# Optimization experiments

Measured on AMD Instinct MI355X. Metric: run time of the kernel, lower is better.

Reference implementation:

```python
import jax, jax.numpy as jnp
import numpy as np

# config
BSZ, L_, DM = 4, 2048, 1024
H, G, P, N, R = 16, 4, 64, 64, 2
RATIO = H // G            # 4
E, K = 64, 2              # kmoe experts / top_k
DPROJ = H * P * 2 + G * N * R * 2 + G * 3  # 3084


def rms(x, w, eps=1e-5):
    return x * jax.lax.rsqrt(jnp.mean(x * x, axis=-1, keepdims=True) + eps) * w


def kron_moe(x, router_w, A_e, B_e, scale, bias, d1, d2, o1, o2, k):
    # x: [..., d1*d2] -> [..., o1*o2]
    orig = x.shape
    xf = x.reshape(-1, d1 * d2)
    logits = xf @ router_w.T                       # [T, E]
    vals, idx = jax.lax.top_k(logits, k)           # [T, k]
    probs = jax.nn.softmax(vals, axis=-1)
    xs = xf.reshape(-1, d1, d2)
    # Y[t,k,o,p] = sum_ij A[t,k,o,i] x[t,i,j] B[t,k,p,j]
    Y = jnp.einsum('tkoi,tij,tkpj->tkop', A_e[idx], xs, B_e[idx])
    out = jnp.sum(Y * probs[:, :, None, None], axis=1).reshape(orig[:-1] + (o1 * o2,))
    return out * scale + bias


def setup_inputs() -> dict:
    key = jax.random.key(0)
    ks = jax.random.split(key, 12)
    r = lambda k, s, sc: jax.random.normal(k, s, jnp.float32) * sc
    return dict(
        u=jax.random.normal(ks[0], (BSZ, L_, DM), jnp.float32),
        in_proj_w=r(ks[1], (DPROJ, DM), 0.02),
        in_proj_b=jnp.zeros((DPROJ,), jnp.float32),
        xup_router=r(ks[2], (E, P), 0.02),
        xup_A=r(ks[3], (E, 8, 8), 0.1),
        xup_B=r(ks[4], (E, 16, 8), 0.1),
        xup_scale=jnp.ones((1,), jnp.float32),
        xup_bias=jnp.zeros((P * R,), jnp.float32),
        ydown_w=r(ks[5], (P, P * R), 0.02),
        oup_router=r(ks[6], (E, H * P), 0.02),
        oup_A=r(ks[7], (E, 32, 32), 0.05),
        oup_B=r(ks[8], (E, 32, 32), 0.05),
        oup_scale=jnp.ones((1,), jnp.float32),
        oup_bias=jnp.zeros((DM,), jnp.float32),
        theta_log=r(ks[9], (G, N // 2), 1.0),
        D=jnp.ones((H,), jnp.float32),
        normB_w=jnp.ones((N * R,), jnp.float32),
        normC_w=jnp.ones((N * R,), jnp.float32),
        bias_B=jnp.zeros((G, N, R), jnp.float32),
        bias_C=jnp.zeros((G, N, R), jnp.float32),
        pregate_w=jnp.ones((H * P,), jnp.float32),
    )


def reference(u, in_proj_w, in_proj_b, xup_router, xup_A, xup_B, xup_scale, xup_bias,
              ydown_w, oup_router, oup_A, oup_B, oup_scale, oup_bias,
              theta_log, D, normB_w, normC_w, bias_B, bias_C, pregate_w):
    B, L, _ = u.shape
    HP, GNR = H * P, G * N * R
    proj = u @ in_proj_w.T + in_proj_b
    splits = np.cumsum([HP, HP, GNR, GNR, G, G])
    z, x_p, Bp, Cp, dt, A_p, lam = jnp.split(proj, splits, axis=-1)
    dt = jax.nn.softplus(dt)                       # [B,L,G]
    A = -jnp.exp(A_p)                              # [B,L,G]
    theta = jnp.exp(theta_log)                     # [G,N/2]
    Bp = rms(Bp.reshape(B, L, G, N * R), normB_w).reshape(B, L, G, N, R) + bias_B
    Cp = rms(Cp.reshape(B, L, G, N * R), normC_w).reshape(B, L, G, N, R) + bias_C
    angles_g = jnp.cumsum(dt[..., None] * theta[None, None], axis=1)   # [B,L,G,N/2]
    rep = lambda v: jnp.repeat(v, RATIO, axis=2)   # group -> head broadcast
    angles = rep(angles_g)                         # [B,L,H,N/2]
    dt_h = rep(dt[..., None])                      # [B,L,H,1]
    A_h = rep(A[..., None])                        # [B,L,H,1]
    B_h, C_h = rep(Bp), rep(Cp)                    # [B,L,H,N,R]
    cos = jnp.cos(angles)[..., None]
    sin = jnp.sin(angles)[..., None]

    def rotate(v):
        re, im = v[..., 0::2, :], v[..., 1::2, :]
        return jnp.stack([re * cos - im * sin, re * sin + im * cos], axis=-2).reshape(v.shape)

    B_rot, C_rot = rotate(B_h), rotate(C_h)
    x = kron_moe(x_p.reshape(B, L, H, P), xup_router, xup_A, xup_B, xup_scale, xup_bias,
                 8, 8, 8, 16, K).reshape(B, L, H, P, R)
    alpha = jnp.exp(dt_h * A_h)[..., None]         # [B,L,H,1,1]

    mv = lambda v: jnp.moveaxis(v, 1, 0)           # time-major for scan

    def step(h, xs):
        Br, Cr, xt, at, dtt = xs
        in_sig = jnp.einsum('bhnr,bhpr->bhnp', Br, xt)
        h = h * at + dtt[..., None] * in_sig
        y_t = jnp.einsum('bhnp,bhnr->bhpr', h, Cr)
        return h, y_t

    h0 = jnp.zeros((B, H, N, P), u.dtype)
    _, ys = jax.lax.scan(step, h0, (mv(B_rot), mv(C_rot), mv(x), mv(alpha), mv(dt_h)))
    y = jnp.moveaxis(ys, 0, 1)                     # [B,L,H,P,R]
    y = (y.reshape(B, L, H, P * R) @ ydown_w.T).reshape(B, L, H * P)
    y = rms(y + x_p * jnp.repeat(D, P), pregate_w) * jax.nn.sigmoid(z)
    out = kron_moe(y, oup_router, oup_A, oup_B, oup_scale, oup_bias, 32, 32, 32, 32, K)
    return out
```

## Files before the change

### kernel.cpp

```cpp
#include <hip/hip_runtime.h>
#include <hip/hip_bf16.h>
#include <math.h>

namespace {
constexpr int kB = 4, kL = 2048, kDM = 1024;
constexpr int kH = 16, kG = 4;
constexpr int kDPROJ = 3084;
constexpr int COL_Z = 0, COL_XP = 1024, COL_B = 2048, COL_C = 2560, COL_DT = 3072, COL_A = 3076;
constexpr int kTOK = kB * kL;
constexpr int kNC = kL / 64;
constexpr int kNPAD = 3200;
constexpr float kLOG2E = 1.4426950408889634f;
}

typedef __attribute__((ext_vector_type(8))) __bf16 bf16x8;
typedef __attribute__((ext_vector_type(8))) unsigned short u16x8;
typedef __attribute__((ext_vector_type(4))) float f32x4;

#define GLDS16(gp, lp)                                                          \
  __builtin_amdgcn_global_load_lds(                                             \
      (const __attribute__((address_space(1))) void*)(gp),                      \
      (__attribute__((address_space(3))) void*)(lp), 16, 0, 0)

__device__ __forceinline__ unsigned short bf16_rne(float f) {
  unsigned u = __builtin_bit_cast(unsigned, f);
  unsigned r = u + 0x7fffu + ((u >> 16) & 1u);
  return (unsigned short)(r >> 16);
}
__device__ __forceinline__ void split2(float f, unsigned short& h, unsigned short& l) {
  unsigned short hh = bf16_rne(f);
  float hf = __builtin_bit_cast(float, (unsigned)hh << 16);
  h = hh;
  l = bf16_rne(f - hf);
}
__device__ __forceinline__ bf16x8 ldsb8(const unsigned short* p) {
  return __builtin_bit_cast(bf16x8, *(const u16x8*)p);
}

__global__ __launch_bounds__(256) void k_split_u(const float* __restrict__ X,
                                                 unsigned short* __restrict__ hi,
                                                 unsigned short* __restrict__ lo) {
  int i = blockIdx.x * 256 + threadIdx.x;
  float4 x = ((const float4*)X)[i];
  float xs[4] = {x.x, x.y, x.z, x.w};
  ushort4 hv, lv;
  unsigned short hq[4], lq[4];
#pragma unroll
  for (int q = 0; q < 4; ++q) split2(xs[q], hq[q], lq[q]);
  hv.x = hq[0]; hv.y = hq[1]; hv.z = hq[2]; hv.w = hq[3];
  lv.x = lq[0]; lv.y = lq[1]; lv.z = lq[2]; lv.w = lq[3];
  ((ushort4*)hi)[i] = hv;
  ((ushort4*)lo)[i] = lv;
}

__global__ __launch_bounds__(256) void k_split_w(const float* __restrict__ X,
                                                 unsigned short* __restrict__ hi,
                                                 unsigned short* __restrict__ lo) {
  int i = blockIdx.x * 256 + threadIdx.x;
  int row = i >> 8;
  float4 x = make_float4(0.f, 0.f, 0.f, 0.f);
  if (row < kDPROJ) x = ((const float4*)X)[i];
  float xs[4] = {x.x, x.y, x.z, x.w};
  ushort4 hv, lv;
  unsigned short hq[4], lq[4];
#pragma unroll
  for (int q = 0; q < 4; ++q) split2(xs[q], hq[q], lq[q]);
  hv.x = hq[0]; hv.y = hq[1]; hv.z = hq[2]; hv.w = hq[3];
  lv.x = lq[0]; lv.y = lq[1]; lv.z = lq[2]; lv.w = lq[3];
  ((ushort4*)hi)[i] = hv;
  ((ushort4*)lo)[i] = lv;
}

__global__ __launch_bounds__(256) void k_inproj_mfma(
    const unsigned short* __restrict__ Uhi, const unsigned short* __restrict__ Ulo,
    const unsigned short* __restrict__ Whi, const unsigned short* __restrict__ Wlo,
    const float* __restrict__ bias, float* __restrict__ proj) {
  __shared__ unsigned short lds_u[16384];
  const int tid = threadIdx.x;
  const int wave = tid >> 6, lane = tid & 63;
  const int wm = wave >> 1, wn = wave & 1;
  const int row0 = blockIdx.x * 128, col0 = blockIdx.y * 128;
  const int fr = lane & 15, kq = lane >> 4;

  f32x4 acc[4][4];
#pragma unroll
  for (int i = 0; i < 4; ++i)
#pragma unroll
    for (int j = 0; j < 4; ++j) acc[i][j] = (f32x4){0.f, 0.f, 0.f, 0.f};

  const int s0 = wave * 64 + lane;

  for (int k0 = 0; k0 < kDM; k0 += 32) {
#pragma unroll
    for (int q = 0; q < 2; ++q) {
      const int slot = q * 256 + s0;
      const int r = slot >> 2;
      const int ce = ((slot & 3) ^ ((r >> 1) & 3)) * 8;
      const size_t ao = (size_t)(row0 + r) * kDM + k0 + ce;
      const size_t bo = (size_t)(col0 + r) * kDM + k0 + ce;
      const int lb = (q * 256 + wave * 64) * 16;
      GLDS16(Uhi + ao, (char*)lds_u + lb);
      GLDS16(Ulo + ao, (char*)lds_u + 8192 + lb);
      GLDS16(Whi + bo, (char*)lds_u + 16384 + lb);
      GLDS16(Wlo + bo, (char*)lds_u + 24576 + lb);
    }
    __syncthreads();
    bf16x8 ahi[4], alo[4], bhi[4], blo[4];
#pragma unroll
    for (int mi = 0; mi < 4; ++mi) {
      int r = wm * 64 + mi * 16 + fr;
      int off = r * 32 + ((kq ^ ((r >> 1) & 3)) * 8);
      ahi[mi] = ldsb8(lds_u + off);
      alo[mi] = ldsb8(lds_u + 4096 + off);
    }
#pragma unroll
    for (int ni = 0; ni < 4; ++ni) {
      int r = wn * 64 + ni * 16 + fr;
      int off = r * 32 + ((kq ^ ((r >> 1) & 3)) * 8);
      bhi[ni] = ldsb8(lds_u + 8192 + off);
      blo[ni] = ldsb8(lds_u + 12288 + off);
    }
#pragma unroll
    for (int mi = 0; mi < 4; ++mi)
#pragma unroll
      for (int ni = 0; ni < 4; ++ni) {
        acc[mi][ni] = __builtin_amdgcn_mfma_f32_16x16x32_bf16(ahi[mi], bhi[ni], acc[mi][ni], 0, 0, 0);
        acc[mi][ni] = __builtin_amdgcn_mfma_f32_16x16x32_bf16(ahi[mi], blo[ni], acc[mi][ni], 0, 0, 0);
        acc[mi][ni] = __builtin_amdgcn_mfma_f32_16x16x32_bf16(alo[mi], bhi[ni], acc[mi][ni], 0, 0, 0);
      }
    __syncthreads();
  }

  const int orow = row0 + wm * 64, ocol = col0 + wn * 64;
#pragma unroll
  for (int mi = 0; mi < 4; ++mi)
#pragma unroll
    for (int ni = 0; ni < 4; ++ni) {
      int cg = ocol + ni * 16 + fr;
      if (cg < kDPROJ) {
        float bv = bias[cg];
#pragma unroll
        for (int r = 0; r < 4; ++r) {
          int rg = orow + mi * 16 + kq * 4 + r;
          proj[(size_t)rg * kDPROJ + cg] = acc[mi][ni][r] + bv;
        }
      }
    }
}

__global__ __launch_bounds__(256) void k_dtprep(const float* __restrict__ proj,
                                                float* __restrict__ dtg,
                                                float* __restrict__ cumalog,
                                                double* __restrict__ cumdt) {
  int bg = blockIdx.x;
  int b = bg / kG, g = bg % kG;
  int tid = threadIdx.x;
  __shared__ double s_dt[256], s_al[256];
  double loc_dt[8], loc_al[8];
  double sdt = 0.0, sal = 0.0;
#pragma unroll
  for (int q = 0; q < 8; ++q) {
    int t = tid * 8 + q;
    size_t i = (size_t)(b * kL + t) * kDPROJ;
    float rd = proj[i + COL_DT + g];
    float ra = proj[i + COL_A + g];
    float dt = rd > 20.f ? rd : log1pf(expf(rd));
    float al = -expf(ra) * dt;
    dtg[(size_t)(b * kL + t) * kG + g] = dt;
    sdt += (double)dt; loc_dt[q] = sdt;
    sal += (double)al; loc_al[q] = sal;
  }
  s_dt[tid] = sdt; s_al[tid] = sal;
  __syncthreads();
  for (int off = 1; off < 256; off <<= 1) {
    double a = 0.0, c = 0.0;
    if (tid >= off) { a = s_dt[tid - off]; c = s_al[tid - off]; }
    __syncthreads();
    s_dt[tid] += a; s_al[tid] += c;
    __syncthreads();
  }
  double base_dt = tid ? s_dt[tid - 1] : 0.0;
  double base_al = tid ? s_al[tid - 1] : 0.0;
#pragma unroll
  for (int q = 0; q < 8; ++q) {
    int t = tid * 8 + q;
    size_t idx = (size_t)(b * kL + t) * kG + g;
    cumdt[idx] = base_dt + loc_dt[q];
    cumalog[idx] = (float)(base_al + loc_al[q]);
  }
}

__global__ __launch_bounds__(256) void k_angles(const double* __restrict__ cumdt,
                                                const float* __restrict__ theta_log,
                                                float* __restrict__ cs_tab) {
  int idx = blockIdx.x * 256 + threadIdx.x;
  int tok = idx >> 7, gk = idx & 127, g = gk >> 5, k = gk & 31;
  double theta = exp((double)theta_log[g * 32 + k]);
  double ang = theta * cumdt[(size_t)tok * kG + g];
  const double twopi = 6.283185307179586476925286766559;
  double rem = ang - floor(ang / twopi) * twopi;
  cs_tab[(size_t)idx * 2] = cosf((float)rem);
  cs_tab[(size_t)idx * 2 + 1] = sinf((float)rem);
}

__global__ __launch_bounds__(256) void k_rotate(float* __restrict__ proj,
                                                const float* __restrict__ cs_tab,
                                                const float* __restrict__ normB_w,
                                                const float* __restrict__ normC_w,
                                                const float* __restrict__ bias_B,
                                                const float* __restrict__ bias_C) {
  int tok = blockIdx.x;
  int tid = threadIdx.x;
  __shared__ float buf[256];
  __shared__ float red[4];
  size_t rowoff = (size_t)tok * kDPROJ;
  int half = tid >> 7;
  int j = tid & 127;
  int wave = tid >> 6;
  for (int g = 0; g < kG; ++g) {
    int col = (half ? COL_C : COL_B) + g * 128 + j;
    float v = proj[rowoff + col];
    float ss = v * v;
    for (int o = 1; o < 64; o <<= 1) ss += __shfl_xor(ss, o);
    if ((tid & 63) == 0) red[wave] = ss;
    __syncthreads();
    float tot = red[half * 2] + red[half * 2 + 1];
    float scale = rsqrtf(tot / 128.f + 1e-5f);
    const float* nw = half ? normC_w : normB_w;
    const float* bb = half ? bias_C : bias_B;
    float nv = v * scale * nw[j] + bb[g * 128 + j];
    buf[tid] = nv;
    __syncthreads();
    float other = buf[tid ^ 2];
    int n = j >> 1, k = n >> 1;
    bool isRe = (n & 1) == 0;
    const float* cs = cs_tab + (((size_t)tok * kG + g) * 32 + k) * 2;
    float cc = cs[0], sn = cs[1];
    float out = isRe ? (nv * cc - other * sn) : (other * sn + nv * cc);
    proj[rowoff + col] = out;
    __syncthreads();
  }
}

__global__ __launch_bounds__(256) void k_xup(const float* __restrict__ proj,
                                             const float* __restrict__ router,
                                             const float* __restrict__ Ae,
                                             const float* __restrict__ Be,
                                             const float* __restrict__ scale_,
                                             const float* __restrict__ bias_,
                                             float* __restrict__ xmoe) {
  int wave = threadIdx.x >> 6, lane = threadIdx.x & 63;
  int unit = blockIdx.x * 4 + wave;
  int tok = unit >> 4, h = unit & 15;
  __shared__ float xs_all[4][64];
  __shared__ float Rs[64][65];
  for (int m = threadIdx.x; m < 64 * 64; m += 256) Rs[m >> 6][m & 63] = router[m];
  float xv = proj[(size_t)tok * kDPROJ + COL_XP + h * 64 + lane];
  xs_all[wave][lane] = xv;
  __syncthreads();
  const float* xs = xs_all[wave];
  double accd = 0.0;
#pragma unroll
  for (int d = 0; d < 64; ++d) accd += (double)Rs[lane][d] * (double)xs[d];
  float logit = (float)accd;
  float v1 = logit; int i1 = lane;
  for (int o = 1; o < 64; o <<= 1) {
    float vv = __shfl_xor(v1, o); int ii = __shfl_xor(i1, o);
    if (vv > v1 || (vv == v1 && ii < i1)) { v1 = vv; i1 = ii; }
  }
  float lm = (lane == i1) ? -INFINITY : logit;
  float v2 = lm; int i2 = lane;
  for (int o = 1; o < 64; o <<= 1) {
    float vv = __shfl_xor(v2, o); int ii = __shfl_xor(i2, o);
    if (vv > v2 || (vv == v2 && ii < i2)) { v2 = vv; i2 = ii; }
  }
  float e12 = expf(v2 - v1);
  float p1 = 1.f / (1.f + e12), p2 = e12 / (1.f + e12);
  float out0 = 0.f, out1 = 0.f;
#pragma unroll
  for (int kk = 0; kk < 2; ++kk) {
    int e = kk ? i2 : i1;
    float pw = kk ? p2 : p1;
    const float* A = Ae + (size_t)e * 64;
    const float* Bm = Be + (size_t)e * 128;
#pragma unroll
    for (int hlf = 0; hlf < 2; ++hlf) {
      int c = lane + hlf * 64;
      int o = c >> 4, p = c & 15;
      float y = 0.f;
#pragma unroll
      for (int i = 0; i < 8; ++i) {
        float t = 0.f;
#pragma unroll
        for (int jj = 0; jj < 8; ++jj) t += xs[i * 8 + jj] * Bm[p * 8 + jj];
        y += A[o * 8 + i] * t;
      }
      if (hlf) out1 += pw * y; else out0 += pw * y;
    }
  }
  float sc = scale_[0];
  size_t ob = (size_t)unit * 128;
  xmoe[ob + lane] = out0 * sc + bias_[lane];
  xmoe[ob + lane + 64] = out1 * sc + bias_[lane + 64];
}

__global__ __launch_bounds__(256) void k_passA(const float* __restrict__ proj,
                                               const float* __restrict__ xmoe,
                                               const float* __restrict__ dtg,
                                               const float* __restrict__ cumalog,
                                               float* __restrict__ hstate) {
  int bid = blockIdx.x;
  int c = bid & 31, h = (bid >> 5) & 15, b = bid >> 9, g = h >> 2;
  int tid = threadIdx.x;
  __shared__ float Bs[128][65];
  __shared__ float Xs[128][65];
  __shared__ float wv[64];
  int base = c * 64;
  size_t tok0 = (size_t)b * kL + base;
  if (tid < 64) {
    float ca_last = cumalog[(tok0 + 63) * kG + g];
    float ca_s = cumalog[(tok0 + tid) * kG + g];
    float dt = dtg[(tok0 + tid) * kG + g];
    wv[tid] = expf(ca_last - ca_s) * dt;
  }
  __syncthreads();
  for (int m = tid; m < 8192; m += 256) {
    int s = m >> 7, j = m & 127;
    float bval = proj[(tok0 + s) * kDPROJ + COL_B + g * 128 + j];
    Bs[s * 2 + (j & 1)][j >> 1] = bval * wv[s];
    float xval = xmoe[((tok0 + s) * kH + h) * (size_t)128 + j];
    Xs[s * 2 + (j & 1)][j >> 1] = xval;
  }
  __syncthreads();
  int tx = tid & 15, ty = tid >> 4;
  float acc[4][4];
#pragma unroll
  for (int i = 0; i < 4; ++i)
#pragma unroll
    for (int j = 0; j < 4; ++j) acc[i][j] = 0.f;
  for (int k = 0; k < 128; ++k) {
    float a[4], bv[4];
#pragma unroll
    for (int q = 0; q < 4; ++q) a[q] = Bs[k][ty * 4 + q];
#pragma unroll
    for (int q = 0; q < 4; ++q) bv[q] = Xs[k][tx * 4 + q];
#pragma unroll
    for (int i = 0; i < 4; ++i)
#pragma unroll
      for (int j = 0; j < 4; ++j) acc[i][j] += a[i] * bv[j];
  }
  float* out = hstate + (size_t)bid * 4096;
#pragma unroll
  for (int i = 0; i < 4; ++i)
#pragma unroll
    for (int j = 0; j < 4; ++j)
      out[(ty * 4 + i) * 64 + tx * 4 + j] = acc[i][j];
}

__global__ __launch_bounds__(256) void k_passB(float* __restrict__ hstate,
                                               const float* __restrict__ cumalog) {
  int bh = blockIdx.x;
  int b = bh >> 4, h = bh & 15, g = h >> 2;
  int tid = threadIdx.x;
  float hrun[16];
#pragma unroll
  for (int q = 0; q < 16; ++q) hrun[q] = 0.f;
  float* Hbase = hstate + (size_t)bh * 32 * 4096;
  for (int c = 0; c < 32; ++c) {
    float ca_last = cumalog[((size_t)b * kL + c * 64 + 63) * kG + g];
    float ca_prev = c ? cumalog[((size_t)b * kL + c * 64 - 1) * kG + g] : 0.f;
    float Dc = expf(ca_last - ca_prev);
    float* Hc = Hbase + (size_t)c * 4096;
#pragma unroll
    for (int q = 0; q < 16; ++q) {
      int idx = tid + q * 256;
      float local = Hc[idx];
      Hc[idx] = hrun[q];
      hrun[q] = Dc * hrun[q] + local;
    }
  }
}

namespace {
constexpr int SC = 72;
constexpr int SG = 136;
constexpr int SH = 72;
constexpr int SW = 66;
}
__global__ __launch_bounds__(256) void k_passC(const float* __restrict__ proj,
                                               const float* __restrict__ xmoe,
                                               const float* __restrict__ dtg,
                                               const float* __restrict__ cumalog,
                                               const float* __restrict__ hstate,
                                               const float* __restrict__ ydown,
                                               float* __restrict__ outY) {
  __shared__ __align__(16) char smem[162560];
  unsigned short* sCh = (unsigned short*)smem;
  unsigned short* sCl = sCh + 128 * SC;
  unsigned short* sBh = (unsigned short*)(smem + 36864);
  unsigned short* sBl = sBh + 128 * SC;
  float*          sW  = (float*)(smem + 73728);
  unsigned short* sHh = (unsigned short*)(smem + 73728);
  unsigned short* sHl = sHh + 64 * SH;
  unsigned short* sGh = (unsigned short*)(smem + 92160);
  unsigned short* sGl = sGh + 128 * SG;
  float* sca  = (float*)(smem + 161792);
  float* sdts = sca + 64;
  float* selx = sdts + 64;
  unsigned short* sXh  = (unsigned short*)smem;
  unsigned short* sXl  = sXh + 64 * SG;
  unsigned short* sWdh = (unsigned short*)(smem + 36864);
  unsigned short* sWdl = sWdh + 64 * SG;
  unsigned short* sYh  = (unsigned short*)(smem + 92160);
  unsigned short* sYl  = sYh + 64 * SG;

  int bid = blockIdx.x;
  int c = bid & 31, h = (bid >> 5) & 15, b = bid >> 9, g = h >> 2;
  int tid = threadIdx.x;
  const int wave = tid >> 6, lane = tid & 63;
  const int fr = lane & 15, kq = lane >> 4;
  int base = c * 64;
  size_t tok0 = (size_t)b * kL + base;
  size_t projBase = tok0 * kDPROJ;

  if (tid < 64) {
    float ca_prev = base ? cumalog[(tok0 - 1) * kG + g] : 0.f;
    float ca_t = cumalog[(tok0 + tid) * kG + g];
    sca[tid] = ca_t;
    sdts[tid] = dtg[(tok0 + tid) * kG + g];
    selx[tid] = exp2f((ca_t - ca_prev) * kLOG2E);
  }
  for (int m = tid; m < 8192; m += 256) {
    int s = m >> 7, j = m & 127;
    int row = s * 2 + (j & 1), col = j >> 1;
    unsigned short hh, ll;
    float cv = proj[projBase + (size_t)s * kDPROJ + COL_C + g * 128 + j];
    split2(cv, hh, ll);
    sCh[row * SC + col] = hh; sCl[row * SC + col] = ll;
    float bv = proj[projBase + (size_t)s * kDPROJ + COL_B + g * 128 + j];
    split2(bv, hh, ll);
    sBh[row * SC + col] = hh; sBl[row * SC + col] = ll;
  }
  __syncthreads();

  for (int m = tid; m < 4096; m += 256) {
    int t = m >> 6, s = m & 63;
    float w = (s <= t) ? sdts[s] * exp2f((sca[t] - sca[s]) * kLOG2E) : 0.f;
    sW[t * SW + s] = w;
  }
  const int rowA0 = wave * 32;
  f32x4 gacc[2][8];
#pragma unroll
  for (int i = 0; i < 2; ++i)
#pragma unroll
    for (int j = 0; j < 8; ++j) gacc[i][j] = (f32x4){0.f, 0.f, 0.f, 0.f};
#pragma unroll
  for (int ks = 0; ks < 2; ++ks) {
    int kb = ks * 32 + kq * 8;
    bf16x8 ah[2], al[2];
#pragma unroll
    for (int mi = 0; mi < 2; ++mi) {
      int off = (rowA0 + mi * 16 + fr) * SC + kb;
      ah[mi] = ldsb8(sCh + off);
      al[mi] = ldsb8(sCl + off);
    }
#pragma unroll
    for (int ni = 0; ni < 8; ++ni) {
      int off = (ni * 16 + fr) * SC + kb;
      bf16x8 bh = ldsb8(sBh + off);
      bf16x8 bl = ldsb8(sBl + off);
#pragma unroll
      for (int mi = 0; mi < 2; ++mi) {
        gacc[mi][ni] = __builtin_amdgcn_mfma_f32_16x16x32_bf16(ah[mi], bh, gacc[mi][ni], 0, 0, 0);
        gacc[mi][ni] = __builtin_amdgcn_mfma_f32_16x16x32_bf16(ah[mi], bl, gacc[mi][ni], 0, 0, 0);
        gacc[mi][ni] = __builtin_amdgcn_mfma_f32_16x16x32_bf16(al[mi], bh, gacc[mi][ni], 0, 0, 0);
      }
    }
  }
  __syncthreads();

#pragma unroll
  for (int mi = 0; mi < 2; ++mi)
#pragma unroll
    for (int ni = 0; ni < 8; ++ni) {
      int colg = ni * 16 + fr;
      int s = colg >> 1;
#pragma unroll
      for (int r = 0; r < 4; ++r) {
        int rowg = rowA0 + mi * 16 + kq * 4 + r;
        int t = rowg >> 1;
        float gm = gacc[mi][ni][r] * sW[t * SW + s];
        unsigned short hh, ll;
        split2(gm, hh, ll);
        sGh[rowg * SG + colg] = hh;
        sGl[rowg * SG + colg] = ll;
      }
    }
  __syncthreads();

  for (int m = tid; m < 4096; m += 256) {
    int n = m >> 6, p = m & 63;
    float v = hstate[(size_t)bid * 4096 + m];
    unsigned short hh, ll;
    split2(v, hh, ll);
    sHh[p * SH + n] = hh;
    sHl[p * SH + n] = ll;
  }
  __syncthreads();

  f32x4 yac[2][4];
#pragma unroll
  for (int i = 0; i < 2; ++i)
#pragma unroll
    for (int j = 0; j < 4; ++j) yac[i][j] = (f32x4){0.f, 0.f, 0.f, 0.f};
#pragma unroll
  for (int ks = 0; ks < 2; ++ks) {
    int kb = ks * 32 + kq * 8;
    bf16x8 ah[2], al[2];
#pragma unroll
    for (int mi = 0; mi < 2; ++mi) {
      int off = (rowA0 + mi * 16 + fr) * SC + kb;
      ah[mi] = ldsb8(sCh + off);
      al[mi] = ldsb8(sCl + off);
    }
#pragma unroll
    for (int ni = 0; ni < 4; ++ni) {
      int off = (ni * 16 + fr) * SH + kb;
      bf16x8 bh = ldsb8(sHh + off);
      bf16x8 bl = ldsb8(sHl + off);
#pragma unroll
      for (int mi = 0; mi < 2; ++mi) {
        yac[mi][ni] = __builtin_amdgcn_mfma_f32_16x16x32_bf16(ah[mi], bh, yac[mi][ni], 0, 0, 0);
        yac[mi][ni] = __builtin_amdgcn_mfma_f32_16x16x32_bf16(ah[mi], bl, yac[mi][ni], 0, 0, 0);
        yac[mi][ni] = __builtin_amdgcn_mfma_f32_16x16x32_bf16(al[mi], bh, yac[mi][ni], 0, 0, 0);
      }
    }
  }
#pragma unroll
  for (int mi = 0; mi < 2; ++mi)
#pragma unroll
    for (int r = 0; r < 4; ++r) {
      int t = (rowA0 + mi * 16 + kq * 4 + r) >> 1;
      float e = selx[t];
#pragma unroll
      for (int ni = 0; ni < 4; ++ni) yac[mi][ni][r] *= e;
    }
  __syncthreads();

  for (int m = tid; m < 8192; m += 256) {
    int s = m >> 7, j = m & 127;
    float xv = xmoe[((tok0 + s) * kH + h) * (size_t)128 + j];
    int p = j >> 1, cc = s * 2 + (j & 1);
    unsigned short hh, ll;
    split2(xv, hh, ll);
    sXh[p * SG + cc] = hh; sXl[p * SG + cc] = ll;
    float wv = ydown[m];
    split2(wv, hh, ll);
    sWdh[(m >> 7) * SG + (m & 127)] = hh;
    sWdl[(m >> 7) * SG + (m & 127)] = ll;
  }
  __syncthreads();

#pragma unroll
  for (int ks = 0; ks < 4; ++ks) {
    int kb = ks * 32 + kq * 8;
    bf16x8 ah[2], al[2];
#pragma unroll
    for (int mi = 0; mi < 2; ++mi) {
      int off = (rowA0 + mi * 16 + fr) * SG + kb;
      ah[mi] = ldsb8(sGh + off);
      al[mi] = ldsb8(sGl + off);
    }
#pragma unroll
    for (int ni = 0; ni < 4; ++ni) {
      int off = (ni * 16 + fr) * SG + kb;
      bf16x8 bh = ldsb8(sXh + off);
      bf16x8 bl = ldsb8(sXl + off);
#pragma unroll
      for (int mi = 0; mi < 2; ++mi) {
        yac[mi][ni] = __builtin_amdgcn_mfma_f32_16x16x32_bf16(ah[mi], bh, yac[mi][ni], 0, 0, 0);
        yac[mi][ni] = __builtin_amdgcn_mfma_f32_16x16x32_bf16(ah[mi], bl, yac[mi][ni], 0, 0, 0);
        yac[mi][ni] = __builtin_amdgcn_mfma_f32_16x16x32_bf16(al[mi], bh, yac[mi][ni], 0, 0, 0);
      }
    }
  }
  __syncthreads();

#pragma unroll
  for (int mi = 0; mi < 2; ++mi)
#pragma unroll
    for (int ni = 0; ni < 4; ++ni)
#pragma unroll
      for (int r = 0; r < 4; ++r) {
        int rowg = rowA0 + mi * 16 + kq * 4 + r;
        int t = rowg >> 1, rr = rowg & 1;
        int p = ni * 16 + fr;
        unsigned short hh, ll;
        split2(yac[mi][ni][r], hh, ll);
        sYh[t * SG + p * 2 + rr] = hh;
        sYl[t * SG + p * 2 + rr] = ll;
      }
  __syncthreads();

  f32x4 zac[4];
#pragma unroll
  for (int j = 0; j < 4; ++j) zac[j] = (f32x4){0.f, 0.f, 0.f, 0.f};
#pragma unroll
  for (int ks = 0; ks < 4; ++ks) {
    int kb = ks * 32 + kq * 8;
    int offA = (wave * 16 + fr) * SG + kb;
    bf16x8 ah = ldsb8(sYh + offA);
    bf16x8 al = ldsb8(sYl + offA);
#pragma unroll
    for (int ni = 0; ni < 4; ++ni) {
      int off = (ni * 16 + fr) * SG + kb;
      bf16x8 bh = ldsb8(sWdh + off);
      bf16x8 bl = ldsb8(sWdl + off);
      zac[ni] = __builtin_amdgcn_mfma_f32_16x16x32_bf16(ah, bh, zac[ni], 0, 0, 0);
      zac[ni] = __builtin_amdgcn_mfma_f32_16x16x32_bf16(ah, bl, zac[ni], 0, 0, 0);
      zac[ni] = __builtin_amdgcn_mfma_f32_16x16x32_bf16(al, bh, zac[ni], 0, 0, 0);
    }
  }
#pragma unroll
  for (int ni = 0; ni < 4; ++ni)
#pragma unroll
    for (int r = 0; r < 4; ++r) {
      int t = wave * 16 + kq * 4 + r;
      int o = ni * 16 + fr;
      outY[(tok0 + t) * (size_t)1024 + h * 64 + o] = zac[ni][r];
    }
}

__global__ __launch_bounds__(256) void k_gate(float* __restrict__ y,
                                              const float* __restrict__ proj,
                                              const float* __restrict__ Dv,
                                              const float* __restrict__ pregate_w) {
  int tok = blockIdx.x;
  int tid = threadIdx.x;
  size_t yoff = (size_t)tok * 1024;
  size_t poff = (size_t)tok * kDPROJ;
  __shared__ float red[4];
  float vals[4];
  float ss = 0.f;
#pragma unroll
  for (int q = 0; q < 4; ++q) {
    int j = tid + q * 256;
    float v = y[yoff + j] + proj[poff + COL_XP + j] * Dv[j >> 6];
    vals[q] = v;
    ss += v * v;
  }
  for (int o = 1; o < 64; o <<= 1) ss += __shfl_xor(ss, o);
  if ((tid & 63) == 0) red[tid >> 6] = ss;
  __syncthreads();
  float tot = red[0] + red[1] + red[2] + red[3];
  float scale = rsqrtf(tot / 1024.f + 1e-5f);
#pragma unroll
  for (int q = 0; q < 4; ++q) {
    int j = tid + q * 256;
    float z = proj[poff + COL_Z + j];
    float sig = 1.f / (1.f + expf(-z));
    y[yoff + j] = vals[q] * scale * pregate_w[j] * sig;
  }
}

__global__ __launch_bounds__(256) void k_oup(float* __restrict__ y,
                                             const float* __restrict__ router,
                                             const float* __restrict__ Ae,
                                             const float* __restrict__ Be,
                                             const float* __restrict__ scale_,
                                             const float* __restrict__ bias_) {
  int tok = blockIdx.x;
  int tid = threadIdx.x;
  __shared__ float xs[1024];
  __shared__ float Ts[32][33];
  __shared__ float logits_s[64];
  __shared__ double partial[256];
  size_t yoff = (size_t)tok * 1024;
  for (int m = tid; m < 1024; m += 256) xs[m] = y[yoff + m];
  __syncthreads();
  {
    int e = tid & 63, q = tid >> 6;
    double acc = 0.0;
    const float* rw = router + (size_t)e * 1024 + q * 256;
    const float* xv = xs + q * 256;
    for (int d = 0; d < 256; ++d) acc += (double)rw[d] * (double)xv[d];
    partial[tid] = acc;
  }
  __syncthreads();
  if (tid < 64) {
    double l = partial[tid] + partial[tid + 64] + partial[tid + 128] + partial[tid + 192];
    logits_s[tid] = (float)l;
  }
  __syncthreads();
  float v1 = -INFINITY; int i1 = -1;
  for (int e = 0; e < 64; ++e) { float v = logits_s[e]; if (v > v1) { v1 = v; i1 = e; } }
  float v2 = -INFINITY; int i2 = -1;
  for (int e = 0; e < 64; ++e) { if (e == i1) continue; float v = logits_s[e]; if (v > v2) { v2 = v; i2 = e; } }
  float e12 = expf(v2 - v1);
  float p1 = 1.f / (1.f + e12), p2 = e12 / (1.f + e12);
  float out[4] = {0.f, 0.f, 0.f, 0.f};
  for (int kk = 0; kk < 2; ++kk) {
    int e = kk ? i2 : i1;
    float pw = kk ? p2 : p1;
    const float* A = Ae + (size_t)e * 1024;
    const float* Bm = Be + (size_t)e * 1024;
    __syncthreads();
    for (int m = tid; m < 1024; m += 256) {
      int i = m >> 5, p = m & 31;
      float t = 0.f;
#pragma unroll
      for (int j = 0; j < 32; ++j) t += xs[i * 32 + j] * Bm[p * 32 + j];
      Ts[i][p] = t;
    }
    __syncthreads();
#pragma unroll
    for (int q = 0; q < 4; ++q) {
      int cc = tid + q * 256;
      int o = cc >> 5, p = cc & 31;
      float a2 = 0.f;
#pragma unroll
      for (int i = 0; i < 32; ++i) a2 += A[o * 32 + i] * Ts[i][p];
      out[q] += pw * a2;
    }
  }
  float sc = scale_[0];
#pragma unroll
  for (int q = 0; q < 4; ++q) {
    int cc = tid + q * 256;
    y[yoff + cc] = out[q] * sc + bias_[cc];
  }
}

extern "C" void kernel_launch(void* const* d_in, const int* in_sizes, int n_in,
                              void* d_out, int out_size, void* d_ws, size_t ws_size,
                              hipStream_t stream) {
  const float* u          = (const float*)d_in[0];
  const float* in_proj_w  = (const float*)d_in[1];
  const float* in_proj_b  = (const float*)d_in[2];
  const float* xup_router = (const float*)d_in[3];
  const float* xup_A      = (const float*)d_in[4];
  const float* xup_B      = (const float*)d_in[5];
  const float* xup_scale  = (const float*)d_in[6];
  const float* xup_bias   = (const float*)d_in[7];
  const float* ydown_w    = (const float*)d_in[8];
  const float* oup_router = (const float*)d_in[9];
  const float* oup_A      = (const float*)d_in[10];
  const float* oup_B      = (const float*)d_in[11];
  const float* oup_scale  = (const float*)d_in[12];
  const float* oup_bias   = (const float*)d_in[13];
  const float* theta_log  = (const float*)d_in[14];
  const float* Dv         = (const float*)d_in[15];
  const float* normB_w    = (const float*)d_in[16];
  const float* normC_w    = (const float*)d_in[17];
  const float* bias_B     = (const float*)d_in[18];
  const float* bias_C     = (const float*)d_in[19];
  const float* pregate_w  = (const float*)d_in[20];

  char* ws = (char*)d_ws;
  float* proj = (float*)ws;      ws += (size_t)kTOK * kDPROJ * 4;
  float* dtg = (float*)ws;       ws += (size_t)kTOK * kG * 4;
  float* cumalog = (float*)ws;   ws += (size_t)kTOK * kG * 4;
  double* cumdt = (double*)ws;   ws += (size_t)kTOK * kG * 8;
  float* cs_tab = (float*)ws;    ws += (size_t)kTOK * kG * 32 * 2 * 4;
  float* xmoe = (float*)ws;      ws += (size_t)kTOK * kH * 128 * 4;
  float* hstate = (float*)ws;    ws += (size_t)kB * kH * kNC * 4096 * 4;
  float* outY = (float*)d_out;

  unsigned short* Uhi = (unsigned short*)xmoe;
  unsigned short* Ulo = Uhi + (size_t)kTOK * kDM;
  unsigned short* Whi = Ulo + (size_t)kTOK * kDM;
  unsigned short* Wlo = Whi + (size_t)kNPAD * kDM;

  k_split_u<<<dim3(kTOK * kDM / 4 / 256), dim3(256), 0, stream>>>(u, Uhi, Ulo);
  k_split_w<<<dim3(kNPAD * kDM / 4 / 256), dim3(256), 0, stream>>>(in_proj_w, Whi, Wlo);
  k_inproj_mfma<<<dim3(kTOK / 128, kNPAD / 128), dim3(256), 0, stream>>>(Uhi, Ulo, Whi, Wlo, in_proj_b, proj);
  k_dtprep<<<dim3(kB * kG), dim3(256), 0, stream>>>(proj, dtg, cumalog, cumdt);
  k_angles<<<dim3(kTOK * 128 / 256), dim3(256), 0, stream>>>(cumdt, theta_log, cs_tab);
  k_rotate<<<dim3(kTOK), dim3(256), 0, stream>>>(proj, cs_tab, normB_w, normC_w, bias_B, bias_C);
  k_xup<<<dim3(kTOK * kH / 4), dim3(256), 0, stream>>>(proj, xup_router, xup_A, xup_B, xup_scale, xup_bias, xmoe);
  k_passA<<<dim3(kB * kH * kNC), dim3(256), 0, stream>>>(proj, xmoe, dtg, cumalog, hstate);
  k_passB<<<dim3(kB * kH), dim3(256), 0, stream>>>(hstate, cumalog);
  k_passC<<<dim3(kB * kH * kNC), dim3(256), 0, stream>>>(proj, xmoe, dtg, cumalog, hstate, ydown_w, outY);
  k_gate<<<dim3(kTOK), dim3(256), 0, stream>>>(outY, proj, Dv, pregate_w);
  k_oup<<<dim3(kTOK), dim3(256), 0, stream>>>(outY, oup_router, oup_A, oup_B, oup_scale, oup_bias);
}
```

Measured before the change: 1.061 ms.

## Split output MoE router logits into a tiled batched kernel

Moves the oup router logit computation out of the per-token k_oup kernel into a separate k_logits kernel. That kernel processes 16 tokens per block and stages router and activation tiles in shared memory, so each router row is reused across tokens instead of being reread from global memory for every token. k_oup now only reads the 64 precomputed logits. The change adds one kernel launch and a round trip of the logits through global memory, stored in the reused cs_tab buffer. The double-precision accumulation is kept.

```diff
diff --git a/kernel.cpp b/kernel.cpp
--- a/kernel.cpp
+++ b/kernel.cpp
@@ -663,8 +663,41 @@
   }
 }
 
+__global__ __launch_bounds__(256) void k_logits(const float* __restrict__ y,
+                                                const float* __restrict__ router,
+                                                float* __restrict__ logits) {
+  __shared__ float Yt[16][65];
+  __shared__ float Rt[64][65];
+  int tid = threadIdx.x;
+  int tok0 = blockIdx.x * 16;
+  int t = tid & 15;
+  int e0 = (tid >> 4) * 4;
+  double acc[4] = {0.0, 0.0, 0.0, 0.0};
+  for (int kc = 0; kc < 1024; kc += 64) {
+    for (int m = tid; m < 1024; m += 256) {
+      int tt = m >> 6, c = m & 63;
+      Yt[tt][c] = y[(size_t)(tok0 + tt) * 1024 + kc + c];
+    }
+    for (int m = tid; m < 4096; m += 256) {
+      int ee = m >> 6, c = m & 63;
+      Rt[ee][c] = router[(size_t)ee * 1024 + kc + c];
+    }
+    __syncthreads();
+    for (int c = 0; c < 64; ++c) {
+      float yv = Yt[t][c];
+#pragma unroll
+      for (int i = 0; i < 4; ++i)
+        acc[i] += (double)Rt[e0 + i][c] * (double)yv;
+    }
+    __syncthreads();
+  }
+#pragma unroll
+  for (int i = 0; i < 4; ++i)
+    logits[(size_t)(tok0 + t) * 64 + e0 + i] = (float)acc[i];
+}
+
 __global__ __launch_bounds__(256) void k_oup(float* __restrict__ y,
-                                             const float* __restrict__ router,
+                                             const float* __restrict__ logits,
                                              const float* __restrict__ Ae,
                                              const float* __restrict__ Be,
                                              const float* __restrict__ scale_,
@@ -673,29 +706,15 @@
   int tid = threadIdx.x;
   __shared__ float xs[1024];
   __shared__ float Ts[32][33];
-  __shared__ float logits_s[64];
-  __shared__ double partial[256];
+  __shared__ float lg[64];
   size_t yoff = (size_t)tok * 1024;
   for (int m = tid; m < 1024; m += 256) xs[m] = y[yoff + m];
-  __syncthreads();
-  {
-    int e = tid & 63, q = tid >> 6;
-    double acc = 0.0;
-    const float* rw = router + (size_t)e * 1024 + q * 256;
-    const float* xv = xs + q * 256;
-    for (int d = 0; d < 256; ++d) acc += (double)rw[d] * (double)xv[d];
-    partial[tid] = acc;
-  }
-  __syncthreads();
-  if (tid < 64) {
-    double l = partial[tid] + partial[tid + 64] + partial[tid + 128] + partial[tid + 192];
-    logits_s[tid] = (float)l;
-  }
+  if (tid < 64) lg[tid] = logits[(size_t)tok * 64 + tid];
   __syncthreads();
   float v1 = -INFINITY; int i1 = -1;
-  for (int e = 0; e < 64; ++e) { float v = logits_s[e]; if (v > v1) { v1 = v; i1 = e; } }
+  for (int e = 0; e < 64; ++e) { float v = lg[e]; if (v > v1) { v1 = v; i1 = e; } }
   float v2 = -INFINITY; int i2 = -1;
-  for (int e = 0; e < 64; ++e) { if (e == i1) continue; float v = logits_s[e]; if (v > v2) { v2 = v; i2 = e; } }
+  for (int e = 0; e < 64; ++e) { if (e == i1) continue; float v = lg[e]; if (v > v2) { v2 = v; i2 = e; } }
   float e12 = expf(v2 - v1);
   float p1 = 1.f / (1.f + e12), p2 = e12 / (1.f + e12);
   float out[4] = {0.f, 0.f, 0.f, 0.f};
@@ -766,6 +785,8 @@
   float* hstate = (float*)ws;    ws += (size_t)kB * kH * kNC * 4096 * 4;
   float* outY = (float*)d_out;
 
+  float* logits = cs_tab;
+
   unsigned short* Uhi = (unsigned short*)xmoe;
   unsigned short* Ulo = Uhi + (size_t)kTOK * kDM;
   unsigned short* Whi = Ulo + (size_t)kTOK * kDM;
@@ -782,5 +803,6 @@
   k_passB<<<dim3(kB * kH), dim3(256), 0, stream>>>(hstate, cumalog);
   k_passC<<<dim3(kB * kH * kNC), dim3(256), 0, stream>>>(proj, xmoe, dtg, cumalog, hstate, ydown_w, outY);
   k_gate<<<dim3(kTOK), dim3(256), 0, stream>>>(outY, proj, Dv, pregate_w);
-  k_oup<<<dim3(kTOK), dim3(256), 0, stream>>>(outY, oup_router, oup_A, oup_B, oup_scale, oup_bias);
-}
+  k_logits<<<dim3(kTOK / 16), dim3(256), 0, stream>>>(outY, oup_router, logits);
+  k_oup<<<dim3(kTOK), dim3(256), 0, stream>>>(outY, logits, oup_A, oup_B, oup_scale, oup_bias);
+}
```

Result: faster. 966.0 us (-9.0%).
